# Performance work log

Measured on AMD Instinct MI355X. Metric: run time of the kernel, lower is better.

## Reference

```python
import jax, jax.numpy as jnp
import numpy as np

B, K, N, C, H, D_CA = 64, 75, 2025, 256, 8, 2
HID = 4 * C


def _ln(x, w, b):
    m = x.mean(-1, keepdims=True)
    v = ((x - m) ** 2).mean(-1, keepdims=True)
    return (x - m) / jnp.sqrt(v + 1e-5) * w + b


def setup_inputs() -> dict:
    key = jax.random.key(0)
    ks = jax.random.split(key, 8)
    def w(k, shape):
        return jax.random.normal(k, shape, jnp.float32) * 0.02
    return {
        "x_cls": jax.random.normal(ks[0], (B, K, C), jnp.float32),
        "x_patch": jax.random.normal(ks[1], (B, N, C), jnp.float32),
        "ln1_w": jnp.ones((D_CA, C), jnp.float32),
        "ln1_b": jnp.zeros((D_CA, C), jnp.float32),
        "q_w": w(ks[2], (D_CA, C, C)),
        "k_w": w(ks[3], (D_CA, C, C)),
        "v_w": w(ks[4], (D_CA, C, C)),
        "proj_w": w(ks[5], (D_CA, C, C)),
        "proj_b": jnp.zeros((D_CA, C), jnp.float32),
        "ln2_w": jnp.ones((D_CA, C), jnp.float32),
        "ln2_b": jnp.zeros((D_CA, C), jnp.float32),
        "fc1_w": w(ks[6], (D_CA, HID, C)),
        "fc1_b": jnp.zeros((D_CA, HID), jnp.float32),
        "fc2_w": w(ks[7], (D_CA, C, HID)),
        "fc2_b": jnp.zeros((D_CA, C), jnp.float32),
        "gamma1": jnp.full((D_CA, C), 1e-4, jnp.float32),
        "gamma2": jnp.full((D_CA, C), 1e-4, jnp.float32),
    }


def reference(x_cls, x_patch, ln1_w, ln1_b, q_w, k_w, v_w, proj_w, proj_b,
              ln2_w, ln2_b, fc1_w, fc1_b, fc2_w, fc2_b, gamma1, gamma2):
    hd = C // H
    scale = hd ** -0.5
    for i in range(D_CA):  # fixed depth_CA=2 class-attention blocks
        u = jnp.concatenate([x_cls, x_patch], axis=1)          # (B, K+N, C)
        un = _ln(u, ln1_w[i], ln1_b[i])
        # Class_Attention: queries only from first K tokens, keys/values from all
        q = (un[:, :K] @ q_w[i].T).reshape(B, K, H, hd) * scale
        kk = (un @ k_w[i].T).reshape(B, K + N, H, hd)
        vv = (un @ v_w[i].T).reshape(B, K + N, H, hd)
        attn = jax.nn.softmax(jnp.einsum('bkhd,bnhd->bhkn', q, kk), axis=-1)
        o = jnp.einsum('bhkn,bnhd->bkhd', attn, vv).reshape(B, K, C)
        x_cls = x_cls + gamma1[i] * (o @ proj_w[i].T + proj_b[i])
        # MLP block on class tokens only
        xn = _ln(x_cls, ln2_w[i], ln2_b[i])
        h = jax.nn.gelu(xn @ fc1_w[i].T + fc1_b[i], approximate=False)
        x_cls = x_cls + gamma2[i] * (h @ fc2_w[i].T + fc2_b[i])
    return x_cls
```

## Files before the change

### kernel.cpp

```cpp
#include <hip/hip_runtime.h>
#include <cstdint>
#include <cstddef>

typedef unsigned short u16;
typedef float f32x4 __attribute__((ext_vector_type(4)));
typedef short s16x8 __attribute__((ext_vector_type(8)));
typedef unsigned short u16x4 __attribute__((ext_vector_type(4)));
typedef __bf16 bf16x8 __attribute__((ext_vector_type(8)));

#define DEV static __device__ __forceinline__

DEV u16 f2bf(float f) {
  uint32_t x = __float_as_uint(f);
  return (u16)((x + 0x7fffu + ((x >> 16) & 1u)) >> 16);
}

DEV f32x4 mfma16(bf16x8 a, bf16x8 b, f32x4 c) {
  return __builtin_amdgcn_mfma_f32_16x16x32_bf16(a, b, c, 0, 0, 0);
}

DEV void mfma_bf16_asm(f32x4& acc, s16x8 a, s16x8 b) {
  asm volatile("v_mfma_f32_16x16x32_bf16 %0, %1, %2, %0" : "+v"(acc) : "v"(a), "v"(b));
}

DEV uint32_t pkbf(float lo, float hi) {
  uint32_t r;
  asm("v_cvt_pk_bf16_f32 %0, %1, %2" : "=v"(r) : "v"(lo), "v"(hi));
  return r;
}

__global__ __launch_bounds__(256) void k_prep(
    const float* __restrict__ x_cls, const float* __restrict__ x_patch,
    const float* __restrict__ k_w, const float* __restrict__ v_w,
    const float* __restrict__ q_w, const float* __restrict__ proj_w,
    const float* __restrict__ fc1_w, const float* __restrict__ fc2_w,
    const float* __restrict__ ln1_w, const float* __restrict__ ln1_b,
    const float* __restrict__ ln2_w, const float* __restrict__ ln2_b,
    const float* __restrict__ fc1_b,
    u16* __restrict__ kvp, u16* __restrict__ qp, u16* __restrict__ pjp,
    u16* __restrict__ f1p, u16* __restrict__ f2p,
    float* __restrict__ bias_kv, float* __restrict__ bias_q, float* __restrict__ bias_f1,
    float* __restrict__ xc, u16* __restrict__ nxp) {
  const int jb = blockIdx.x;
  const int lane = threadIdx.x & 63;
  if (jb >= 2736) {
    int wv = (jb - 2736) * 4 + (threadIdx.x >> 6);
    if (wv >= 129600) return;
    float4 v = ((const float4*)(x_patch + (size_t)wv * 256))[lane];
    float s = v.x + v.y + v.z + v.w;
    float q = v.x * v.x + v.y * v.y + v.z * v.z + v.w * v.w;
#pragma unroll
    for (int m = 1; m < 64; m <<= 1) {
      s += __shfl_xor(s, m, 64);
      q += __shfl_xor(q, m, 64);
    }
    float mean = s * (1.f / 256.f);
    float var = q * (1.f / 256.f) - mean * mean;
    float rstd = rsqrtf(var + 1e-5f);
    u16x4 o;
    o[0] = f2bf((v.x - mean) * rstd);
    o[1] = f2bf((v.y - mean) * rstd);
    o[2] = f2bf((v.z - mean) * rstd);
    o[3] = f2bf((v.w - mean) * rstd);
    ((u16x4*)(nxp + (size_t)wv * 256))[lane] = o;
    return;
  }
  if (jb >= 1536) {
    int i = (jb - 1536) * 256 + threadIdx.x;
    ((float4*)xc)[i] = ((const float4*)x_cls)[i];
    return;
  }
  const int layer = jb >= 768 ? 1 : 0;
  const int j = jb - layer * 768;
  const float* W;
  const float* lw = ln1_w + layer * 256;
  const float* lb = ln1_b + layer * 256;
  const float* b0 = nullptr;
  u16* Wout;
  float* bout = nullptr;
  int rowoff;
  if (j < 64)       { W = k_w + layer * 65536;    Wout = kvp + layer * 131072;         bout = bias_kv + layer * 512;       rowoff = j * 4; }
  else if (j < 128) { W = v_w + layer * 65536;    Wout = kvp + layer * 131072 + 65536; bout = bias_kv + layer * 512 + 256; rowoff = (j - 64) * 4; }
  else if (j < 192) { W = q_w + layer * 65536;    Wout = qp + layer * 65536;           bout = bias_q + layer * 256;        rowoff = (j - 128) * 4; }
  else if (j < 448) { W = fc1_w + layer * 262144; lw = ln2_w + layer * 256; lb = ln2_b + layer * 256; b0 = fc1_b + layer * 1024;
                      Wout = f1p + layer * 262144; bout = bias_f1 + layer * 1024;      rowoff = (j - 192) * 4; }
  else if (j < 512) { W = proj_w + layer * 65536; lw = nullptr;                        Wout = pjp + layer * 65536;         rowoff = (j - 448) * 4; }
  else              { W = fc2_w + layer * 262144; lw = nullptr;                        Wout = f2p + layer * 262144;        rowoff = (j - 512) * 4; }
  const int wv = rowoff + (threadIdx.x >> 6);
  float4 w4 = ((const float4*)(W + (size_t)wv * 256))[lane];
  u16x4 o;
  if (lw) {
    float4 s4 = ((const float4*)lw)[lane];
    o[0] = f2bf(w4.x * s4.x); o[1] = f2bf(w4.y * s4.y);
    o[2] = f2bf(w4.z * s4.z); o[3] = f2bf(w4.w * s4.w);
  } else {
    o[0] = f2bf(w4.x); o[1] = f2bf(w4.y); o[2] = f2bf(w4.z); o[3] = f2bf(w4.w);
  }
  ((u16x4*)(Wout + (size_t)wv * 256))[lane] = o;
  if (bout) {
    float4 t4 = ((const float4*)lb)[lane];
    float d = w4.x * t4.x + w4.y * t4.y + w4.z * t4.z + w4.w * t4.w;
#pragma unroll
    for (int m = 1; m < 64; m <<= 1) d += __shfl_xor(d, m, 64);
    if (lane == 0) bout[wv] = (b0 ? b0[wv] : 0.f) + d;
  }
}

__global__ __launch_bounds__(256) void k_norm(const float* __restrict__ src,
                                              u16* __restrict__ out, int ntok) {
  int wv = blockIdx.x * 4 + (threadIdx.x >> 6), lane = threadIdx.x & 63;
  if (wv >= ntok) return;
  float4 v = ((const float4*)(src + (size_t)wv * 256))[lane];
  float s = v.x + v.y + v.z + v.w;
  float q = v.x * v.x + v.y * v.y + v.z * v.z + v.w * v.w;
#pragma unroll
  for (int m = 1; m < 64; m <<= 1) {
    s += __shfl_xor(s, m, 64);
    q += __shfl_xor(q, m, 64);
  }
  float mean = s * (1.f / 256.f);
  float var = q * (1.f / 256.f) - mean * mean;
  float rstd = rsqrtf(var + 1e-5f);
  u16x4 o;
  o[0] = f2bf((v.x - mean) * rstd);
  o[1] = f2bf((v.y - mean) * rstd);
  o[2] = f2bf((v.z - mean) * rstd);
  o[3] = f2bf((v.w - mean) * rstd);
  ((u16x4*)(out + (size_t)wv * 256))[lane] = o;
}

__global__ __launch_bounds__(256) void k_gemm6(const u16* __restrict__ A,
                                               const u16* __restrict__ Bw,
                                               int N, int K, int mode,
                                               int lognby, float scale,
                                               const float* __restrict__ bias,
                                               const float* __restrict__ gamma,
                                               u16* __restrict__ obf,
                                               float* __restrict__ of32) {
  __shared__ __align__(16) char smA[8192];
  __shared__ __align__(16) char smB[16384];
  const int tid = threadIdx.x, lane = tid & 63, wid = tid >> 6;
  const int wm = wid >> 1, wn = wid & 1;
  const int bid = blockIdx.x;
  const int by = bid & ((1 << lognby) - 1), bx = bid >> lognby;
  const int m0 = bx * 64, n0 = by * 128;
  const int g = lane >> 4, l15 = lane & 15;

  f32x4 acc[2][4] = {};

  for (int k0 = 0; k0 < K; k0 += 64) {
#pragma unroll
    for (int c = 0; c < 2; c++) {
      int ee = tid + 256 * c;
      int row = ee >> 3, sl = ee & 7;
      s16x8 av = *(const s16x8*)(A + (size_t)(m0 + row) * K + k0 + sl * 8);
      *(s16x8*)(smA + row * 128 + ((sl * 16) ^ ((row & 7) << 4))) = av;
    }
#pragma unroll
    for (int c = 0; c < 4; c++) {
      int ee = tid + 256 * c;
      int row = ee >> 3, sl = ee & 7;
      s16x8 bv = *(const s16x8*)(Bw + (size_t)(n0 + row) * K + k0 + sl * 8);
      *(s16x8*)(smB + row * 128 + ((sl * 16) ^ ((row & 7) << 4))) = bv;
    }
    __syncthreads();
    s16x8 af[2][2], bfr[4][2];
#pragma unroll
    for (int s = 0; s < 2; s++) {
#pragma unroll
      for (int i = 0; i < 2; i++) {
        int r = wm * 32 + i * 16 + l15;
        af[i][s] = *(const s16x8*)(smA + r * 128 + (((s * 4 + g) * 16) ^ ((r & 7) << 4)));
      }
#pragma unroll
      for (int jj = 0; jj < 4; jj++) {
        int n = wn * 64 + jj * 16 + l15;
        bfr[jj][s] = *(const s16x8*)(smB + n * 128 + (((s * 4 + g) * 16) ^ ((n & 7) << 4)));
      }
    }
#pragma unroll
    for (int s = 0; s < 2; s++)
#pragma unroll
      for (int i = 0; i < 2; i++)
#pragma unroll
        for (int jj = 0; jj < 4; jj++)
          mfma_bf16_asm(acc[i][jj], af[i][s], bfr[jj][s]);
    __syncthreads();
  }
  asm volatile("s_nop 7\n\ts_nop 7" ::: "memory");

#pragma unroll
  for (int i = 0; i < 2; i++) {
#pragma unroll
    for (int jj = 0; jj < 4; jj++) {
      int gmBase = m0 + wm * 32 + i * 16 + g * 4;
      int gn = n0 + wn * 64 + jj * 16 + l15;
      float bs = bias[gn];
#pragma unroll
      for (int r = 0; r < 4; r++) {
        int gm = gmBase + r;
        float v = acc[i][jj][r] + bs;
        if (mode == 1) {
          obf[(size_t)gm * N + gn] = f2bf(v * scale);
        } else if (mode == 2) {
          of32[(size_t)gm * N + gn] += gamma[gn] * v;
        } else {
          obf[(size_t)gm * N + gn] = f2bf(0.5f * v * (1.f + erff(v * 0.70710678118654752f)));
        }
      }
    }
  }
}

__global__ __launch_bounds__(256, 3) void k_fattn(const u16* __restrict__ qb,
                                                  const u16* __restrict__ uncls,
                                                  const u16* __restrict__ nxp,
                                                  const u16* __restrict__ wkv,
                                                  const float* __restrict__ bias_kv,
                                                  u16* __restrict__ obf) {
  __shared__ __align__(16) char arena[50176];
  __shared__ float mlS[4][160];
  const int bid = blockIdx.x;
  const int b = bid & 63, h = bid >> 6;
  const int tid = threadIdx.x, lane = tid & 63, w = tid >> 6;
  const int l15 = lane & 15, g = lane >> 4;

  u16* WL = (u16*)arena;
  char* wb = arena + 32768 + w * 4352;
  uint32_t* KL = (uint32_t*)wb;
  uint32_t* PB = (uint32_t*)wb;
  u16* VL = (u16*)(wb + 2048);

  for (int it = tid; it < 2048; it += 256) {
    int row = it >> 5, c16 = it & 31;
    int srcRow = (row < 32) ? (h * 32 + row) : (256 + h * 32 + (row - 32));
    s16x8 w8 = *(const s16x8*)(wkv + (size_t)srcRow * 256 + c16 * 8);
    *(s16x8*)(WL + row * 256 + (((c16 * 16) ^ ((row & 7) << 4)) >> 1)) = w8;
  }

  float bk[2][4], bvb[2][4];
#pragma unroll
  for (int s2 = 0; s2 < 2; s2++)
#pragma unroll
    for (int r = 0; r < 4; r++) {
      bk[s2][r] = bias_kv[h * 32 + s2 * 16 + 4 * g + r];
      bvb[s2][r] = bias_kv[256 + h * 32 + s2 * 16 + 4 * g + r];
    }

  bf16x8 bq[5];
#pragma unroll
  for (int qt = 0; qt < 5; qt++) {
    int q = qt * 16 + l15; if (q > 74) q = 74;
    s16x8 qv = *(const s16x8*)(qb + (size_t)(b * 75 + q) * 256 + h * 32 + g * 8);
    bq[qt] = __builtin_bit_cast(bf16x8, qv);
  }

  f32x4 acc[5][2] = {};
  float mlc[5], llc[5];
#pragma unroll
  for (int qt = 0; qt < 5; qt++) { mlc[qt] = -1e30f; llc[qt] = 0.f; }

  __syncthreads();

  const int xw = (l15 & 7) << 4;
  const int xK = ((l15 >> 2) & 3) << 2;

  for (int tt = w; tt < 66; tt += 4) {
    const int t0 = tt * 32;
    int tA = t0 + l15;      if (tA > 2099) tA = 2099;
    int tB = t0 + 16 + l15; if (tB > 2099) tB = 2099;
    const u16* rowA = (tA < 75) ? uncls + ((size_t)b * 75 + tA) * 256
                                : nxp + ((size_t)b * 2025 + (tA - 75)) * 256;
    const u16* rowB = (tB < 75) ? uncls + ((size_t)b * 75 + tB) * 256
                                : nxp + ((size_t)b * 2025 + (tB - 75)) * 256;

    f32x4 aK[2][2] = {}, aV[2][2] = {};
    __builtin_amdgcn_s_setprio(1);
#pragma unroll
    for (int ks = 0; ks < 8; ks++) {
      bf16x8 nA = __builtin_bit_cast(bf16x8, *(const s16x8*)(rowA + ks * 32 + g * 8));
      bf16x8 nB = __builtin_bit_cast(bf16x8, *(const s16x8*)(rowB + ks * 32 + g * 8));
      const int cb = (ks * 64 + g * 16) ^ xw;
      bf16x8 k0 = __builtin_bit_cast(bf16x8, *(const s16x8*)(WL + l15 * 256 + (cb >> 1)));
      bf16x8 k1 = __builtin_bit_cast(bf16x8, *(const s16x8*)(WL + (16 + l15) * 256 + (cb >> 1)));
      bf16x8 w0 = __builtin_bit_cast(bf16x8, *(const s16x8*)(WL + (32 + l15) * 256 + (cb >> 1)));
      bf16x8 w1 = __builtin_bit_cast(bf16x8, *(const s16x8*)(WL + (48 + l15) * 256 + (cb >> 1)));
      aK[0][0] = mfma16(k0, nA, aK[0][0]);
      aK[0][1] = mfma16(k0, nB, aK[0][1]);
      aK[1][0] = mfma16(k1, nA, aK[1][0]);
      aK[1][1] = mfma16(k1, nB, aK[1][1]);
      aV[0][0] = mfma16(w0, nA, aV[0][0]);
      aV[0][1] = mfma16(w0, nB, aV[0][1]);
      aV[1][0] = mfma16(w1, nA, aV[1][0]);
      aV[1][1] = mfma16(w1, nB, aV[1][1]);
    }
    __builtin_amdgcn_s_setprio(0);

#pragma unroll
    for (int s2 = 0; s2 < 2; s2++)
#pragma unroll
      for (int u = 0; u < 2; u++) {
        const int trow = u * 16 + l15;
        f32x4 kk4 = aK[s2][u];
        uint2 pk2;
        pk2.x = pkbf(kk4[0] + bk[s2][0], kk4[1] + bk[s2][1]);
        pk2.y = pkbf(kk4[2] + bk[s2][2], kk4[3] + bk[s2][3]);
        *(uint2*)&KL[trow * 16 + ((s2 * 8 + 2 * g) ^ xK)] = pk2;
        f32x4 vv4 = aV[s2][u];
        uint2 pv2;
        pv2.x = pkbf(vv4[0] + bvb[s2][0], vv4[1] + bvb[s2][1]);
        pv2.y = pkbf(vv4[2] + bvb[s2][2], vv4[3] + bvb[s2][3]);
        *(uint2*)&VL[trow * 36 + ((s2 * 16 + 4 * g) ^ (u << 4))] = pv2;
      }

    uint4 ka = *(const uint4*)&KL[l15 * 16 + ((4 * g) ^ xK)];
    uint4 kb = *(const uint4*)&KL[(16 + l15) * 16 + ((4 * g) ^ xK)];
    bf16x8 bA = __builtin_bit_cast(bf16x8, ka);
    bf16x8 bB = __builtin_bit_cast(bf16x8, kb);
    s16x8 v0, v1;
#pragma unroll
    for (int e = 0; e < 8; e++) {
      int vrow = 8 * g + e;
      int mx = vrow & 16;
      v0[e] = (short)VL[vrow * 36 + (l15 ^ mx)];
      v1[e] = (short)VL[vrow * 36 + ((16 + l15) ^ mx)];
    }
    bf16x8 bv0 = __builtin_bit_cast(bf16x8, v0);
    bf16x8 bv1 = __builtin_bit_cast(bf16x8, v1);

    const bool lastTile = (t0 == 2080);

#pragma unroll
    for (int qt = 0; qt < 5; qt++) {
      f32x4 z = {0.f, 0.f, 0.f, 0.f};
      f32x4 sA = mfma16(bA, bq[qt], z);
      f32x4 sB = mfma16(bB, bq[qt], z);
      if (lastTile && g >= 1) {
        sB[0] = sB[1] = sB[2] = sB[3] = -1e30f;
      }
      float px = fmaxf(fmaxf(fmaxf(sA[0], sA[1]), fmaxf(sA[2], sA[3])),
                       fmaxf(fmaxf(sB[0], sB[1]), fmaxf(sB[2], sB[3])));
      px = fmaxf(px, __shfl_xor(px, 16, 64));
      px = fmaxf(px, __shfl_xor(px, 32, 64));
      float mq = mlc[qt];
      if (!__all(px <= mq + 8.f)) {
        float mn = fmaxf(mq, px);
        float rs = exp2f(mq - mn);
        mlc[qt] = mn;
        llc[qt] *= rs;
#pragma unroll
        for (int r = 0; r < 4; r++) {
          float rr = __shfl(rs, ((lane >> 4) << 2) + r, 64);
          acc[qt][0][r] *= rr;
          acc[qt][1][r] *= rr;
        }
        mq = mn;
      }
      f32x4 pA, pB;
#pragma unroll
      for (int r = 0; r < 4; r++) {
        pA[r] = exp2f(sA[r] - mq);
        pB[r] = exp2f(sB[r] - mq);
      }
      llc[qt] += pA[0] + pA[1] + pA[2] + pA[3] + pB[0] + pB[1] + pB[2] + pB[3];
      uint32_t* Pu = &PB[l15 * 20];
      Pu[2 * g]     = pkbf(pA[0], pA[1]);
      Pu[2 * g + 1] = pkbf(pA[2], pA[3]);
      Pu[8 + 2 * g]     = pkbf(pB[0], pB[1]);
      Pu[8 + 2 * g + 1] = pkbf(pB[2], pB[3]);
      uint4 pu = *(const uint4*)&PB[l15 * 20 + 4 * g];
      bf16x8 bp = __builtin_bit_cast(bf16x8, pu);
      acc[qt][0] = mfma16(bp, bv0, acc[qt][0]);
      acc[qt][1] = mfma16(bp, bv1, acc[qt][1]);
    }
  }

#pragma unroll
  for (int qt = 0; qt < 5; qt++) {
    float t = llc[qt];
    t += __shfl_xor(t, 16, 64);
    t += __shfl_xor(t, 32, 64);
    llc[qt] = t;
  }
  __syncthreads();
  float* MC = (float*)arena;
#pragma unroll
  for (int qt = 0; qt < 5; qt++)
#pragma unroll
    for (int dh = 0; dh < 2; dh++)
#pragma unroll
      for (int r = 0; r < 4; r++) {
        int q = qt * 16 + 4 * g + r;
        MC[w * 2560 + q * 32 + dh * 16 + l15] = acc[qt][dh][r];
      }
  if (lane < 16) {
#pragma unroll
    for (int qt = 0; qt < 5; qt++) {
      mlS[w][qt * 16 + l15] = mlc[qt];
      mlS[w][80 + qt * 16 + l15] = llc[qt];
    }
  }
  __syncthreads();

  for (int idx = tid; idx < 2400; idx += 256) {
    int q = idx >> 5, d = idx & 31;
    float M = -1e30f;
#pragma unroll
    for (int ww = 0; ww < 4; ww++) M = fmaxf(M, mlS[ww][q]);
    float L = 0.f, O = 0.f;
#pragma unroll
    for (int ww = 0; ww < 4; ww++) {
      float sc = exp2f(mlS[ww][q] - M);
      L += mlS[ww][80 + q] * sc;
      O += MC[ww * 2560 + q * 32 + d] * sc;
    }
    obf[(size_t)(b * 75 + q) * 256 + h * 32 + d] = f2bf(O / L);
  }
}

extern "C" void kernel_launch(void* const* d_in, const int* in_sizes, int n_in,
                              void* d_out, int out_size, void* d_ws, size_t ws_size,
                              hipStream_t stream) {
  const float* x_cls   = (const float*)d_in[0];
  const float* x_patch = (const float*)d_in[1];
  const float* ln1_w   = (const float*)d_in[2];
  const float* ln1_b   = (const float*)d_in[3];
  const float* q_w     = (const float*)d_in[4];
  const float* k_w     = (const float*)d_in[5];
  const float* v_w     = (const float*)d_in[6];
  const float* proj_w  = (const float*)d_in[7];
  const float* proj_b  = (const float*)d_in[8];
  const float* ln2_w   = (const float*)d_in[9];
  const float* ln2_b   = (const float*)d_in[10];
  const float* fc1_w   = (const float*)d_in[11];
  const float* fc1_b   = (const float*)d_in[12];
  const float* fc2_w   = (const float*)d_in[13];
  const float* fc2_b   = (const float*)d_in[14];
  const float* gamma1  = (const float*)d_in[15];
  const float* gamma2  = (const float*)d_in[16];
  float* xc = (float*)d_out;

  char* ws = (char*)d_ws;
  size_t off = 0;
  auto alloc = [&](size_t bytes) {
    char* p = ws + off;
    off += (bytes + 255) & ~(size_t)255;
    return p;
  };
  u16* nxp   = (u16*)alloc(129600ull * 256 * 2);
  u16* uncls = (u16*)alloc(4800ull * 256 * 2);
  u16* qb    = (u16*)alloc(4800ull * 256 * 2);
  u16* ob    = (u16*)alloc(4800ull * 256 * 2);
  u16* xn    = (u16*)alloc(4800ull * 256 * 2);
  u16* hb    = (u16*)alloc(4800ull * 1024 * 2);
  u16* qp    = (u16*)alloc(2ull * 65536 * 2);
  u16* kvp   = (u16*)alloc(2ull * 131072 * 2);
  u16* pjp   = (u16*)alloc(2ull * 65536 * 2);
  u16* f1p   = (u16*)alloc(2ull * 262144 * 2);
  u16* f2p   = (u16*)alloc(2ull * 262144 * 2);
  float* bias_kv = (float*)alloc(2ull * 512 * 4);
  float* bias_q  = (float*)alloc(2ull * 256 * 4);
  float* bias_f1 = (float*)alloc(2ull * 1024 * 4);

  k_prep<<<35136, 256, 0, stream>>>(x_cls, x_patch, k_w, v_w, q_w, proj_w, fc1_w, fc2_w,
                                    ln1_w, ln1_b, ln2_w, ln2_b, fc1_b,
                                    kvp, qp, pjp, f1p, f2p,
                                    bias_kv, bias_q, bias_f1, xc, nxp);

  const float qscale = 0.25503489f;
  for (int i = 0; i < 2; i++) {
    k_norm<<<1200, 256, 0, stream>>>(xc, uncls, 4800);
    k_gemm6<<<150, 256, 0, stream>>>(uncls, qp + i * 65536, 256, 256, 1, 1, qscale,
                                     bias_q + i * 256, nullptr, qb, nullptr);
    k_fattn<<<512, 256, 0, stream>>>(qb, uncls, nxp, kvp + i * 131072,
                                     bias_kv + i * 512, ob);
    k_gemm6<<<150, 256, 0, stream>>>(ob, pjp + i * 65536, 256, 256, 2, 1, 0.f,
                                     proj_b + i * 256, gamma1 + i * 256, nullptr, xc);
    k_norm<<<1200, 256, 0, stream>>>(xc, xn, 4800);
    k_gemm6<<<600, 256, 0, stream>>>(xn, f1p + i * 262144, 1024, 256, 3, 3, 0.f,
                                     bias_f1 + i * 1024, nullptr, hb, nullptr);
    k_gemm6<<<150, 256, 0, stream>>>(hb, f2p + i * 262144, 256, 1024, 2, 1, 0.f,
                                     fc2_b + i * 256, gamma2 + i * 256, nullptr, xc);
  }
}
```

Before: 364.9 us.

## Split attention over key halves with a separate combine kernel

The fused attention kernel now splits the 66 key tiles into two halves, launching 1024 blocks instead of 512. Each block writes its partial output, max and sum to fp32 workspace, and a new combine kernel merges the two halves and writes the bf16 output. The intent is to fill more CUs on a 256-CU part, where 512 blocks leave the GPU underused. In exchange it adds an extra launch, round-trips through global memory, and redundant per-block weight staging. The diff also lowers launch bounds from 3 to 2 blocks per SM, changes the LDS swizzles for K/V, and moves the row-sum reduction into the inner loop.

```diff
diff --git a/kernel.cpp b/kernel.cpp
--- a/kernel.cpp
+++ b/kernel.cpp
@@ -212,18 +212,20 @@
   }
 }
 
-__global__ __launch_bounds__(256, 3) void k_fattn(const u16* __restrict__ qb,
+__global__ __launch_bounds__(256, 2) void k_fattn(const u16* __restrict__ qb,
                                                   const u16* __restrict__ uncls,
                                                   const u16* __restrict__ nxp,
                                                   const u16* __restrict__ wkv,
                                                   const float* __restrict__ bias_kv,
-                                                  u16* __restrict__ obf) {
+                                                  float* __restrict__ pO,
+                                                  float* __restrict__ pml) {
   __shared__ __align__(16) char arena[50176];
   __shared__ float mlS[4][160];
   const int bid = blockIdx.x;
-  const int b = bid & 63, h = bid >> 6;
+  const int b = bid & 63, h = (bid >> 6) & 7, half = bid >> 9;
   const int tid = threadIdx.x, lane = tid & 63, w = tid >> 6;
   const int l15 = lane & 15, g = lane >> 4;
+  const int tbase = half * 33, tend = tbase + 33;
 
   u16* WL = (u16*)arena;
   char* wb = arena + 32768 + w * 4352;
@@ -263,9 +265,9 @@
   __syncthreads();
 
   const int xw = (l15 & 7) << 4;
-  const int xK = ((l15 >> 2) & 3) << 2;
-
-  for (int tt = w; tt < 66; tt += 4) {
+  const int xk = (l15 & 3) << 2;
+
+  for (int tt = tbase + w; tt < tend; tt += 4) {
     const int t0 = tt * 32;
     int tA = t0 + l15;      if (tA > 2099) tA = 2099;
     int tB = t0 + 16 + l15; if (tB > 2099) tB = 2099;
@@ -305,25 +307,23 @@
         uint2 pk2;
         pk2.x = pkbf(kk4[0] + bk[s2][0], kk4[1] + bk[s2][1]);
         pk2.y = pkbf(kk4[2] + bk[s2][2], kk4[3] + bk[s2][3]);
-        *(uint2*)&KL[trow * 16 + ((s2 * 8 + 2 * g) ^ xK)] = pk2;
+        *(uint2*)&KL[trow * 16 + ((s2 * 8 + 2 * g) ^ ((trow & 3) << 2))] = pk2;
         f32x4 vv4 = aV[s2][u];
-        uint2 pv2;
-        pv2.x = pkbf(vv4[0] + bvb[s2][0], vv4[1] + bvb[s2][1]);
-        pv2.y = pkbf(vv4[2] + bvb[s2][2], vv4[3] + bvb[s2][3]);
-        *(uint2*)&VL[trow * 36 + ((s2 * 16 + 4 * g) ^ (u << 4))] = pv2;
-      }
-
-    uint4 ka = *(const uint4*)&KL[l15 * 16 + ((4 * g) ^ xK)];
-    uint4 kb = *(const uint4*)&KL[(16 + l15) * 16 + ((4 * g) ^ xK)];
+        uint32_t pv0 = pkbf(vv4[0] + bvb[s2][0], vv4[1] + bvb[s2][1]);
+        uint32_t pv1 = pkbf(vv4[2] + bvb[s2][2], vv4[3] + bvb[s2][3]);
+        *(uint32_t*)&VL[trow * 36 + s2 * 16 + 4 * g] = pv0;
+        *(uint32_t*)&VL[trow * 36 + s2 * 16 + 4 * g + 2] = pv1;
+      }
+
+    uint4 ka = *(const uint4*)&KL[l15 * 16 + ((4 * g) ^ xk)];
+    uint4 kb = *(const uint4*)&KL[(16 + l15) * 16 + ((4 * g) ^ xk)];
     bf16x8 bA = __builtin_bit_cast(bf16x8, ka);
     bf16x8 bB = __builtin_bit_cast(bf16x8, kb);
     s16x8 v0, v1;
 #pragma unroll
     for (int e = 0; e < 8; e++) {
-      int vrow = 8 * g + e;
-      int mx = vrow & 16;
-      v0[e] = (short)VL[vrow * 36 + (l15 ^ mx)];
-      v1[e] = (short)VL[vrow * 36 + ((16 + l15) ^ mx)];
+      v0[e] = (short)VL[(8 * g + e) * 36 + l15];
+      v1[e] = (short)VL[(8 * g + e) * 36 + 16 + l15];
     }
     bf16x8 bv0 = __builtin_bit_cast(bf16x8, v0);
     bf16x8 bv1 = __builtin_bit_cast(bf16x8, v1);
@@ -362,7 +362,10 @@
         pA[r] = exp2f(sA[r] - mq);
         pB[r] = exp2f(sB[r] - mq);
       }
-      llc[qt] += pA[0] + pA[1] + pA[2] + pA[3] + pB[0] + pB[1] + pB[2] + pB[3];
+      float ps = pA[0] + pA[1] + pA[2] + pA[3] + pB[0] + pB[1] + pB[2] + pB[3];
+      ps += __shfl_xor(ps, 16, 64);
+      ps += __shfl_xor(ps, 32, 64);
+      llc[qt] += ps;
       uint32_t* Pu = &PB[l15 * 20];
       Pu[2 * g]     = pkbf(pA[0], pA[1]);
       Pu[2 * g + 1] = pkbf(pA[2], pA[3]);
@@ -375,13 +378,6 @@
     }
   }
 
-#pragma unroll
-  for (int qt = 0; qt < 5; qt++) {
-    float t = llc[qt];
-    t += __shfl_xor(t, 16, 64);
-    t += __shfl_xor(t, 32, 64);
-    llc[qt] = t;
-  }
   __syncthreads();
   float* MC = (float*)arena;
 #pragma unroll
@@ -402,18 +398,44 @@
   }
   __syncthreads();
 
+  if (tid < 75) {
+    float M = -1e30f;
+#pragma unroll
+    for (int ww = 0; ww < 4; ww++) M = fmaxf(M, mlS[ww][tid]);
+    float L = 0.f;
+#pragma unroll
+    for (int ww = 0; ww < 4; ww++) L += mlS[ww][80 + tid] * exp2f(mlS[ww][tid] - M);
+    pml[(size_t)bid * 160 + tid] = M;
+    pml[(size_t)bid * 160 + 80 + tid] = L;
+  }
+  for (int idx = tid; idx < 2400; idx += 256) {
+    int q = idx >> 5;
+    float M = -1e30f;
+#pragma unroll
+    for (int ww = 0; ww < 4; ww++) M = fmaxf(M, mlS[ww][q]);
+    float O = 0.f;
+#pragma unroll
+    for (int ww = 0; ww < 4; ww++) O += MC[ww * 2560 + q * 32 + (idx & 31)] * exp2f(mlS[ww][q] - M);
+    pO[(size_t)bid * 2400 + idx] = O;
+  }
+}
+
+__global__ __launch_bounds__(256) void k_acomb(const float* __restrict__ pO,
+                                               const float* __restrict__ pml,
+                                               u16* __restrict__ obf) {
+  const int bid = blockIdx.x;
+  const int b = bid & 63, h = bid >> 6;
+  const int tid = threadIdx.x;
   for (int idx = tid; idx < 2400; idx += 256) {
     int q = idx >> 5, d = idx & 31;
-    float M = -1e30f;
-#pragma unroll
-    for (int ww = 0; ww < 4; ww++) M = fmaxf(M, mlS[ww][q]);
-    float L = 0.f, O = 0.f;
-#pragma unroll
-    for (int ww = 0; ww < 4; ww++) {
-      float sc = exp2f(mlS[ww][q] - M);
-      L += mlS[ww][80 + q] * sc;
-      O += MC[ww * 2560 + q * 32 + d] * sc;
-    }
+    float m0 = pml[(size_t)bid * 160 + q];
+    float l0 = pml[(size_t)bid * 160 + 80 + q];
+    float m1 = pml[(size_t)(bid + 512) * 160 + q];
+    float l1 = pml[(size_t)(bid + 512) * 160 + 80 + q];
+    float M = fmaxf(m0, m1);
+    float s0 = exp2f(m0 - M), s1 = exp2f(m1 - M);
+    float L = l0 * s0 + l1 * s1;
+    float O = pO[(size_t)bid * 2400 + idx] * s0 + pO[(size_t)(bid + 512) * 2400 + idx] * s1;
     obf[(size_t)(b * 75 + q) * 256 + h * 32 + d] = f2bf(O / L);
   }
 }
@@ -461,6 +483,8 @@
   float* bias_kv = (float*)alloc(2ull * 512 * 4);
   float* bias_q  = (float*)alloc(2ull * 256 * 4);
   float* bias_f1 = (float*)alloc(2ull * 1024 * 4);
+  float* pO  = (float*)alloc(1024ull * 2400 * 4);
+  float* pml = (float*)alloc(1024ull * 160 * 4);
 
   k_prep<<<35136, 256, 0, stream>>>(x_cls, x_patch, k_w, v_w, q_w, proj_w, fc1_w, fc2_w,
                                     ln1_w, ln1_b, ln2_w, ln2_b, fc1_b,
@@ -472,8 +496,9 @@
     k_norm<<<1200, 256, 0, stream>>>(xc, uncls, 4800);
     k_gemm6<<<150, 256, 0, stream>>>(uncls, qp + i * 65536, 256, 256, 1, 1, qscale,
                                      bias_q + i * 256, nullptr, qb, nullptr);
-    k_fattn<<<512, 256, 0, stream>>>(qb, uncls, nxp, kvp + i * 131072,
-                                     bias_kv + i * 512, ob);
+    k_fattn<<<1024, 256, 0, stream>>>(qb, uncls, nxp, kvp + i * 131072,
+                                      bias_kv + i * 512, pO, pml);
+    k_acomb<<<512, 256, 0, stream>>>(pO, pml, ob);
     k_gemm6<<<150, 256, 0, stream>>>(ob, pjp + i * 65536, 256, 256, 2, 1, 0.f,
                                      proj_b + i * 256, gamma1 + i * 256, nullptr, xc);
     k_norm<<<1200, 256, 0, stream>>>(xc, xn, 4800);
```

Result: no change. 357.9 us (-1.9%).
